# Kernel tuning notes

Hardware: AMD Instinct MI355X
Metric: run time of the kernel (lower is better)

Reference implementation:

```python
import jax, jax.numpy as jnp
import numpy as np
from jax import lax

B, C_IN, H, W = 4, 256, 64, 64
C_OUT = 512
KEY_DIM = C_OUT // 2   # 256
VAL_DIM = C_OUT // 2   # 256
HEADS = 8
EPS = 1e-5


def _conv(x, w, stride, pad):
    return lax.conv_general_dilated(
        x, w, (stride, stride), [(pad, pad), (pad, pad)],
        dimension_numbers=('NCHW', 'OIHW', 'NCHW'))


def setup_inputs() -> dict:
    key = jax.random.key(0)
    ks = jax.random.split(key, 10)
    x = jax.random.normal(ks[0], (B, C_IN, H, W), jnp.float32)
    bn_gamma = jax.random.uniform(ks[1], (C_IN,), jnp.float32, 0.5, 1.5)
    bn_beta = jax.random.normal(ks[2], (C_IN,), jnp.float32) * 0.1
    bn_mean = jax.random.normal(ks[3], (C_IN,), jnp.float32) * 0.1
    bn_var = jax.random.uniform(ks[4], (C_IN,), jnp.float32, 0.5, 1.5)
    w_short = jax.random.normal(ks[5], (C_OUT, C_IN, 3, 3), jnp.float32) * (1.0 / np.sqrt(C_IN * 9))
    wq = jax.random.normal(ks[6], (KEY_DIM, C_IN, 1, 1), jnp.float32) * (1.0 / np.sqrt(C_IN))
    wk = jax.random.normal(ks[7], (KEY_DIM, C_IN, 1, 1), jnp.float32) * (1.0 / np.sqrt(C_IN))
    wv = jax.random.normal(ks[8], (VAL_DIM, C_IN, 1, 1), jnp.float32) * (1.0 / np.sqrt(C_IN))
    wo = jax.random.normal(ks[9], (C_OUT, VAL_DIM, 1, 1), jnp.float32) * (1.0 / np.sqrt(VAL_DIM))
    return dict(x=x, bn_gamma=bn_gamma, bn_beta=bn_beta, bn_mean=bn_mean,
                bn_var=bn_var, w_short=w_short, wq=wq, wk=wk, wv=wv, wo=wo)


def reference(x, bn_gamma, bn_beta, bn_mean, bn_var, w_short, wq, wk, wv, wo):
    # BatchNorm (inference: running stats) + ReLU, fused elementwise chain
    inv = bn_gamma / jnp.sqrt(bn_var + EPS)
    h = jax.nn.relu((x - bn_mean[None, :, None, None]) * inv[None, :, None, None]
                    + bn_beta[None, :, None, None])

    # Projection shortcut: 3x3 conv, stride 2, pad 1, no bias -> [B, C_OUT, H/2, W/2]
    shortcut = _conv(h, w_short, 2, 1)

    # DOWN attention: queries at stride 2 (downsampled grid), keys/values at full res
    q = _conv(h, wq, 2, 0)   # [B, KEY_DIM, H/2, W/2]
    k = _conv(h, wk, 1, 0)   # [B, KEY_DIM, H, W]
    v = _conv(h, wv, 1, 0)   # [B, VAL_DIM, H, W]

    Ho, Wo = H // 2, W // 2
    dk = KEY_DIM // HEADS
    dv = VAL_DIM // HEADS
    Nq, Nk = Ho * Wo, H * W

    qh = q.reshape(B, HEADS, dk, Nq)
    kh = k.reshape(B, HEADS, dk, Nk)
    vh = v.reshape(B, HEADS, dv, Nk)

    scale = 1.0 / np.sqrt(dk)
    scores = jnp.einsum('bhdq,bhdk->bhqk', qh, kh) * scale  # [B,H,Nq,Nk]
    attn = jax.nn.softmax(scores, axis=-1)                  # use_softmax=True
    out = jnp.einsum('bhqk,bhdk->bhdq', attn, vh)           # [B,H,dv,Nq]
    out = out.reshape(B, VAL_DIM, Ho, Wo)
    out = _conv(out, wo, 1, 0)                              # [B, C_OUT, Ho, Wo]

    return shortcut + out
```

## Files before the change

### kernel.cpp

```cpp
#include <hip/hip_runtime.h>

#define BB    4
#define CIN   256
#define NPIX  4096
#define COUT  512
#define KD    256
#define HEADS 8
#define NQ    1024
#define NK    4096
#define EPSV  1e-5f
#define QSCALE (0.17677669529663687f * 1.4426950408889634f)

using short8 = __attribute__((ext_vector_type(8))) short;
using f32x4  = __attribute__((ext_vector_type(4))) float;

__device__ __forceinline__ float b2f(unsigned u){ return __uint_as_float(u << 16); }
__device__ __forceinline__ unsigned short f2b(float f){
  unsigned u = __float_as_uint(f);
  return (unsigned short)((u + 0x7fffu + ((u >> 16) & 1u)) >> 16);
}
__device__ __forceinline__ float bnrelu(float xv, float inv, float mu, float bt){
  return fmaxf((xv - mu) * inv + bt, 0.0f);
}
__device__ __forceinline__ unsigned pkbf(float lo, float hi){
  unsigned a = __float_as_uint(lo) + 0x8000u;
  unsigned b = __float_as_uint(hi) + 0x8000u;
  return __builtin_amdgcn_perm(b, a, 0x07060302u);
}
__device__ __forceinline__ unsigned cvtpk(float lo, float hi){
  unsigned r;
  asm("v_cvt_pk_bf16_f32 %0, %1, %2" : "=v"(r) : "v"(lo), "v"(hi));
  return r;
}

#define WF_K  2560
#define WF_E  (512*2560)

__global__ __launch_bounds__(256) void prep_all(
    const float* __restrict__ x, const float* __restrict__ gam,
    const float* __restrict__ bet, const float* __restrict__ mea,
    const float* __restrict__ var,
    const float* __restrict__ wsh, const float* __restrict__ wq,
    const float* __restrict__ wk,  const float* __restrict__ wv,
    const float* __restrict__ wo,
    unsigned short* __restrict__ h_t, unsigned short* __restrict__ W2){
  __shared__ unsigned short T[64][264];
  const int blk = blockIdx.x;
  const int t = threadIdx.x;
  if (blk < 832){
    if (blk < 512){
      float* R = (float*)&T[0][0];
      const float* src = wsh + (size_t)blk * 2304;
      #pragma unroll
      for (int i = 0; i < 9; ++i) R[i * 256 + t] = src[i * 256 + t];
      __syncthreads();
      unsigned short* dst = W2 + (size_t)blk * WF_K;
      #pragma unroll
      for (int i = 0; i < 9; ++i){
        int kp = i * 256 + t;
        int tap = kp >> 8, ci = kp & 255;
        dst[kp] = f2b(R[ci * 9 + tap]);
      }
    } else if (blk < 704){
      int idx = (blk - 512) * 1024 + t * 4;
      float4 v;
      if (idx < 65536){
        v = *(const float4*)(wq + idx);
        v.x *= QSCALE; v.y *= QSCALE; v.z *= QSCALE; v.w *= QSCALE;
      } else if (idx < 2*65536){ v = *(const float4*)(wk + idx - 65536);
      } else {                   v = *(const float4*)(wv + idx - 2*65536); }
      uint2 pk;
      pk.x = (unsigned)f2b(v.x) | ((unsigned)f2b(v.y) << 16);
      pk.y = (unsigned)f2b(v.z) | ((unsigned)f2b(v.w) << 16);
      *(uint2*)(W2 + WF_E + idx) = pk;
    } else {
      int idx = (blk - 704) * 1024 + t * 4;
      int m = idx >> 8, c = idx & 255;
      float4 v = *(const float4*)(wo + idx);
      uint2 pk;
      pk.x = (unsigned)f2b(v.x) | ((unsigned)f2b(v.y) << 16);
      pk.y = (unsigned)f2b(v.z) | ((unsigned)f2b(v.w) << 16);
      *(uint2*)(W2 + (size_t)m * WF_K + 2304 + c) = pk;
    }
    return;
  }
  const int lin = blk - 832;
  const int b = lin >> 6;
  const int pix0 = (lin & 63) * 64;
  const int w = t >> 6, lane = t & 63;
  for (int cc = 0; cc < 32; ++cc){
    int c0 = cc * 8 + w * 2;
    float i0 = gam[c0]   * rsqrtf(var[c0]   + EPSV), mu0 = mea[c0],   bt0 = bet[c0];
    float i1 = gam[c0+1] * rsqrtf(var[c0+1] + EPSV), mu1 = mea[c0+1], bt1 = bet[c0+1];
    float v0 = bnrelu(x[((size_t)(b*CIN + c0  ))*NPIX + pix0 + lane], i0, mu0, bt0);
    float v1 = bnrelu(x[((size_t)(b*CIN + c0+1))*NPIX + pix0 + lane], i1, mu1, bt1);
    *(unsigned*)&T[lane][c0] = pkbf(v0, v1);
  }
  __syncthreads();
  int p = t >> 2;
  unsigned short* dst = h_t + ((size_t)b * NPIX + pix0 + p) * CIN;
  #pragma unroll
  for (int i = 0; i < 8; ++i){
    int coff = i * 32 + (t & 3) * 8;
    *(uint4*)(dst + coff) = *(const uint4*)&T[p][coff];
  }
}

__global__ __launch_bounds__(256) void qkv_gemm(
    const unsigned short* __restrict__ Wkv,
    const unsigned short* __restrict__ Wq,
    const unsigned short* __restrict__ h_t,
    unsigned short* __restrict__ ktg,
    unsigned short* __restrict__ vtg,
    unsigned short* __restrict__ qt){
  __shared__ unsigned short As[64][72];
  __shared__ unsigned short Bs[128][72];
  const int b = blockIdx.z;
  const int t = threadIdx.x;
  const int w = t >> 6, lane = t & 63, col = lane & 15, quad = lane >> 4;
  const int wm = w & 1, wn = w >> 1;

  if (blockIdx.y < 8){
    const int m0 = blockIdx.y * 64;
    const bool isv = m0 >= 256;
    const int n0 = blockIdx.x * 128;
    f32x4 acc[2][4];
    #pragma unroll
    for (int i = 0; i < 2; ++i)
      #pragma unroll
      for (int j = 0; j < 4; ++j) acc[i][j] = (f32x4){0.f,0.f,0.f,0.f};
    const int am = t >> 2, ak = (t & 3) * 8;
    const int bn = t >> 1, bkh = (t & 1) * 16;
    const size_t browbase = ((size_t)b * NPIX + (n0 + bn)) * CIN;

    uint4 av0 = *(const uint4*)(Wkv + (size_t)(m0 + am) * 256 + ak);
    uint4 av1 = *(const uint4*)(Wkv + (size_t)(m0 + am) * 256 + 32 + ak);
    uint4 bv0 = *(const uint4*)(h_t + browbase + bkh);
    uint4 bv1 = *(const uint4*)(h_t + browbase + bkh + 8);
    uint4 bv2 = *(const uint4*)(h_t + browbase + 32 + bkh);
    uint4 bv3 = *(const uint4*)(h_t + browbase + 32 + bkh + 8);

    for (int k0 = 0; k0 < 256; k0 += 64){
      *(uint4*)&As[am][ak]           = av0;
      *(uint4*)&As[am][32 + ak]      = av1;
      *(uint4*)&Bs[bn][bkh]          = bv0;
      *(uint4*)&Bs[bn][bkh + 8]      = bv1;
      *(uint4*)&Bs[bn][32 + bkh]     = bv2;
      *(uint4*)&Bs[bn][32 + bkh + 8] = bv3;
      __syncthreads();
      if (k0 + 64 < 256){
        av0 = *(const uint4*)(Wkv + (size_t)(m0 + am) * 256 + k0 + 64 + ak);
        av1 = *(const uint4*)(Wkv + (size_t)(m0 + am) * 256 + k0 + 96 + ak);
        bv0 = *(const uint4*)(h_t + browbase + k0 + 64 + bkh);
        bv1 = *(const uint4*)(h_t + browbase + k0 + 64 + bkh + 8);
        bv2 = *(const uint4*)(h_t + browbase + k0 + 96 + bkh);
        bv3 = *(const uint4*)(h_t + browbase + k0 + 96 + bkh + 8);
      }
      #pragma unroll
      for (int h = 0; h < 2; ++h){
        short8 af[2], bf[4];
        af[0] = *(const short8*)&As[wm * 32 +      col][h * 32 + quad * 8];
        af[1] = *(const short8*)&As[wm * 32 + 16 + col][h * 32 + quad * 8];
        #pragma unroll
        for (int j = 0; j < 4; ++j)
          bf[j] = *(const short8*)&Bs[wn * 64 + j * 16 + col][h * 32 + quad * 8];
        if (!isv){
          #pragma unroll
          for (int i = 0; i < 2; ++i)
            #pragma unroll
            for (int j = 0; j < 4; ++j)
              acc[i][j] = __builtin_amdgcn_mfma_f32_16x16x32_bf16(af[i], bf[j], acc[i][j], 0, 0, 0);
        } else {
          #pragma unroll
          for (int i = 0; i < 2; ++i)
            #pragma unroll
            for (int j = 0; j < 4; ++j)
              acc[i][j] = __builtin_amdgcn_mfma_f32_16x16x32_bf16(bf[j], af[i], acc[i][j], 0, 0, 0);
        }
      }
      __syncthreads();
    }

    if (!isv){
      int head = (m0 + wm * 32) >> 5;
      #pragma unroll
      for (int i = 0; i < 2; ++i){
        int d0 = i * 16 + quad * 4;
        #pragma unroll
        for (int j = 0; j < 4; ++j){
          int n = n0 + wn * 64 + j * 16 + col;
          uint2 pk;
          pk.x = pkbf(acc[i][j][0], acc[i][j][1]);
          pk.y = pkbf(acc[i][j][2], acc[i][j][3]);
          *(uint2*)(ktg + ((size_t)(b * HEADS + head) * NK + n) * 32 + d0) = pk;
        }
      }
    } else {
      int head = ((m0 - 256) + wm * 32) >> 5;
      #pragma unroll
      for (int i = 0; i < 2; ++i){
        int d = i * 16 + col;
        #pragma unroll
        for (int j = 0; j < 4; ++j){
          int nb = n0 + wn * 64 + j * 16 + quad * 4;
          size_t addr = (((size_t)(b * HEADS + head) * 128 + (nb >> 5)) * 32 + d) * 32 + (nb & 31);
          uint2 pk;
          pk.x = pkbf(acc[i][j][0], acc[i][j][1]);
          pk.y = pkbf(acc[i][j][2], acc[i][j][3]);
          *(uint2*)(vtg + addr) = pk;
        }
      }
    }
    return;
  }

  const int lin = (blockIdx.y - 8) * 32 + blockIdx.x;
  const int m0 = (lin >> 4) * 64;
  const int n0 = (lin & 15) * 64;
  f32x4 acc[2][2];
  #pragma unroll
  for (int i = 0; i < 2; ++i)
    #pragma unroll
    for (int j = 0; j < 2; ++j) acc[i][j] = (f32x4){0.f,0.f,0.f,0.f};
  const int am = t >> 2, ak = (t & 3) * 8;
  const int bn = t >> 2, bk = (t & 3) * 8;
  int n = n0 + bn;
  const size_t browbase = ((size_t)b * NPIX + (((n >> 5) << 7) + ((n & 31) << 1))) * CIN;

  uint4 av0 = *(const uint4*)(Wq + (size_t)(m0 + am) * 256 + ak);
  uint4 av1 = *(const uint4*)(Wq + (size_t)(m0 + am) * 256 + 32 + ak);
  uint4 bv0 = *(const uint4*)(h_t + browbase + bk);
  uint4 bv1 = *(const uint4*)(h_t + browbase + 32 + bk);

  for (int k0 = 0; k0 < 256; k0 += 64){
    *(uint4*)&As[am][ak]      = av0;
    *(uint4*)&As[am][32 + ak] = av1;
    *(uint4*)&Bs[bn][bk]      = bv0;
    *(uint4*)&Bs[bn][32 + bk] = bv1;
    __syncthreads();
    if (k0 + 64 < 256){
      av0 = *(const uint4*)(Wq + (size_t)(m0 + am) * 256 + k0 + 64 + ak);
      av1 = *(const uint4*)(Wq + (size_t)(m0 + am) * 256 + k0 + 96 + ak);
      bv0 = *(const uint4*)(h_t + browbase + k0 + 64 + bk);
      bv1 = *(const uint4*)(h_t + browbase + k0 + 96 + bk);
    }
    #pragma unroll
    for (int h = 0; h < 2; ++h){
      short8 af[2], bf[2];
      af[0] = *(const short8*)&As[wm * 32 +      col][h * 32 + quad * 8];
      af[1] = *(const short8*)&As[wm * 32 + 16 + col][h * 32 + quad * 8];
      bf[0] = *(const short8*)&Bs[wn * 32 +      col][h * 32 + quad * 8];
      bf[1] = *(const short8*)&Bs[wn * 32 + 16 + col][h * 32 + quad * 8];
      #pragma unroll
      for (int i = 0; i < 2; ++i)
        #pragma unroll
        for (int j = 0; j < 2; ++j)
          acc[i][j] = __builtin_amdgcn_mfma_f32_16x16x32_bf16(af[i], bf[j], acc[i][j], 0, 0, 0);
    }
    __syncthreads();
  }

  int head = (m0 + wm * 32) >> 5;
  #pragma unroll
  for (int i = 0; i < 2; ++i){
    int d0 = i * 16 + quad * 4;
    #pragma unroll
    for (int j = 0; j < 2; ++j){
      int nn = n0 + wn * 32 + j * 16 + col;
      uint2 pk;
      pk.x = pkbf(acc[i][j][0], acc[i][j][1]);
      pk.y = pkbf(acc[i][j][2], acc[i][j][3]);
      *(uint2*)(qt + ((size_t)(b * HEADS + head) * NQ + nn) * 32 + d0) = pk;
    }
  }
}

__global__ __launch_bounds__(256) void scwo_gemm(
    const unsigned short* __restrict__ Wf,
    const unsigned short* __restrict__ h_t,
    const unsigned short* __restrict__ aot,
    float* __restrict__ outf){
  const int b  = blockIdx.z;
  const int m0 = blockIdx.y * 64;
  const int n0 = blockIdx.x * 64;
  const int t  = threadIdx.x;
  const int w = t >> 6, lane = t & 63, col = lane & 15, quad = lane >> 4;
  const int wm = w & 1, wn = w >> 1;
  __shared__ unsigned short As[64][72];
  __shared__ unsigned short Bs[64][72];
  f32x4 acc[2][2];
  #pragma unroll
  for (int i = 0; i < 2; ++i)
    #pragma unroll
    for (int j = 0; j < 2; ++j) acc[i][j] = (f32x4){0.f,0.f,0.f,0.f};
  const int am = t >> 2, ak = (t & 3) * 8;
  const int bn = t >> 2, bk = (t & 3) * 8;
  const int n = n0 + bn;
  const int oy = n >> 5, ox = n & 31;
  const size_t aobase = ((size_t)b * NQ + n) * KD;

  auto loadB = [&](int k0) -> uint4 {
    if (k0 < 2304){
      int tap = k0 >> 8;
      int ky = tap / 3, kx = tap - ky * 3;
      int iy = 2 * oy + ky - 1, ix = 2 * ox + kx - 1;
      if (((unsigned)iy < 64u) && ((unsigned)ix < 64u))
        return *(const uint4*)(h_t + ((size_t)b * NPIX + iy * 64 + ix) * CIN + (k0 & 255) + bk);
      return make_uint4(0,0,0,0);
    }
    return *(const uint4*)(aot + aobase + (k0 - 2304) + bk);
  };

  uint4 av0 = *(const uint4*)(Wf + (size_t)(m0 + am) * WF_K + ak);
  uint4 av1 = *(const uint4*)(Wf + (size_t)(m0 + am) * WF_K + 32 + ak);
  uint4 bv0 = loadB(0);
  uint4 bv1 = loadB(32);

  for (int k0 = 0; k0 < WF_K; k0 += 64){
    *(uint4*)&As[am][ak]      = av0;
    *(uint4*)&As[am][32 + ak] = av1;
    *(uint4*)&Bs[bn][bk]      = bv0;
    *(uint4*)&Bs[bn][32 + bk] = bv1;
    __syncthreads();
    if (k0 + 64 < WF_K){
      av0 = *(const uint4*)(Wf + (size_t)(m0 + am) * WF_K + k0 + 64 + ak);
      av1 = *(const uint4*)(Wf + (size_t)(m0 + am) * WF_K + k0 + 96 + ak);
      bv0 = loadB(k0 + 64);
      bv1 = loadB(k0 + 96);
    }
    #pragma unroll
    for (int h = 0; h < 2; ++h){
      short8 af[2], bf[2];
      af[0] = *(const short8*)&As[wm * 32 +      col][h * 32 + quad * 8];
      af[1] = *(const short8*)&As[wm * 32 + 16 + col][h * 32 + quad * 8];
      bf[0] = *(const short8*)&Bs[wn * 32 +      col][h * 32 + quad * 8];
      bf[1] = *(const short8*)&Bs[wn * 32 + 16 + col][h * 32 + quad * 8];
      #pragma unroll
      for (int i = 0; i < 2; ++i)
        #pragma unroll
        for (int j = 0; j < 2; ++j)
          acc[i][j] = __builtin_amdgcn_mfma_f32_16x16x32_bf16(bf[j], af[i], acc[i][j], 0, 0, 0);
    }
    __syncthreads();
  }

  #pragma unroll
  for (int i = 0; i < 2; ++i){
    int co = m0 + wm * 32 + i * 16 + col;
    #pragma unroll
    for (int j = 0; j < 2; ++j){
      int nb = n0 + wn * 32 + j * 16 + quad * 4;
      float4 o;
      o.x = acc[i][j][0]; o.y = acc[i][j][1];
      o.z = acc[i][j][2]; o.w = acc[i][j][3];
      *(float4*)(outf + ((size_t)(b * COUT + co)) * NQ + nb) = o;
    }
  }
}

__global__ __launch_bounds__(512) void attn12(
    const unsigned short* __restrict__ qt,
    const unsigned short* __restrict__ ktg,
    const unsigned short* __restrict__ vtg,
    float* __restrict__ po,
    float* __restrict__ pl){
  __shared__ unsigned short KV[2][8192];
  const int bid = blockIdx.x;
  const int xcd = bid & 7, idx = bid >> 3;
  const int bh = xcd * 4 + (idx & 3);
  const int qg = (idx >> 2) & 7;
  const int kh = idx >> 5;
  const int t = threadIdx.x;
  const int w = t >> 6, lane = t & 63, col = lane & 15, quad = lane >> 4;
  const int q = (qg * 8 + w) * 16 + col;

  short8 qf = *(const short8*)(qt + ((size_t)bh * NQ + q) * 32 + quad * 8);
  const unsigned short* kb = ktg + (size_t)bh * NK * 32;
  const unsigned short* vb = vtg + (size_t)bh * 128 * 1024;

  const int sg = (w & 3) >> 1, sf = w & 1;
  const size_t ksrc = (size_t)(32 * sg + 16 * sf + col) * 32 + quad * 8;
  const size_t vsrc = (size_t)sg * 1024 + (size_t)(16 * sf + col) * 32 + quad * 8;
  const unsigned short* sb = ((w < 4) ? kb + ksrc : vb + vsrc) + (size_t)kh * 65536;
  unsigned short* ddst = &KV[0][w * 512 + lane * 8 + ((w < 4) ? 0 : 2048)];

  f32x4 O0 = {0.f,0.f,0.f,0.f}, O1 = {0.f,0.f,0.f,0.f}, l4 = {0.f,0.f,0.f,0.f};
  const short8 ones = {0x3F80,0x3F80,0x3F80,0x3F80,0x3F80,0x3F80,0x3F80,0x3F80};

  *(uint4*)ddst          = *(const uint4*)sb;
  *(uint4*)(ddst + 2048) = *(const uint4*)(sb + 2048);
  __syncthreads();

  for (int s = 0; s < 16; ++s){
    const int cur = s & 1;
    uint4 n1, n2;
    if (s + 1 < 16){
      size_t soff = (size_t)(s + 1) * 4096;
      n1 = *(const uint4*)(sb + soff);
      n2 = *(const uint4*)(sb + soff + 2048);
    }
    #pragma unroll
    for (int g = 0; g < 4; ++g){
      const unsigned short* Kp = &KV[cur][g * 1024];
      short8 kf0 = *(const short8*)(Kp +       lane * 8);
      short8 kf1 = *(const short8*)(Kp + 512 + lane * 8);
      f32x4 z = {0.f,0.f,0.f,0.f};
      f32x4 slo = __builtin_amdgcn_mfma_f32_16x16x32_bf16(kf0, qf, z, 0, 0, 0);
      f32x4 shi = __builtin_amdgcn_mfma_f32_16x16x32_bf16(kf1, qf, z, 0, 0, 0);

      unsigned x0 = cvtpk(__builtin_amdgcn_exp2f(slo[0]), __builtin_amdgcn_exp2f(slo[1]));
      unsigned x1 = cvtpk(__builtin_amdgcn_exp2f(slo[2]), __builtin_amdgcn_exp2f(slo[3]));
      unsigned y0 = cvtpk(__builtin_amdgcn_exp2f(shi[0]), __builtin_amdgcn_exp2f(shi[1]));
      unsigned y1 = cvtpk(__builtin_amdgcn_exp2f(shi[2]), __builtin_amdgcn_exp2f(shi[3]));
      asm("v_permlane32_swap_b32 %0, %1" : "+v"(x0), "+v"(y0));
      asm("v_permlane32_swap_b32 %0, %1" : "+v"(x1), "+v"(y1));
      asm("v_permlane16_swap_b32 %0, %1" : "+v"(x0), "+v"(y0));
      asm("v_permlane16_swap_b32 %0, %1" : "+v"(x1), "+v"(y1));
      unsigned f[4] = {x0, x1, y0, y1};
      short8 pf;
      memcpy(&pf, f, 16);

      const unsigned short* Vp = &KV[cur][4096 + g * 1024];
      short8 vf0 = *(const short8*)(Vp +       lane * 8);
      short8 vf1 = *(const short8*)(Vp + 512 + lane * 8);
      O0 = __builtin_amdgcn_mfma_f32_16x16x32_bf16(vf0, pf, O0, 0, 0, 0);
      O1 = __builtin_amdgcn_mfma_f32_16x16x32_bf16(vf1, pf, O1, 0, 0, 0);
      l4 = __builtin_amdgcn_mfma_f32_16x16x32_bf16(ones, pf, l4, 0, 0, 0);
    }
    if (s + 1 < 16){
      *(uint4*)(ddst + (size_t)(cur ^ 1) * 8192)        = n1;
      *(uint4*)(ddst + 2048 + (size_t)(cur ^ 1) * 8192) = n2;
    }
    __syncthreads();
  }

  float* pob = po + (((size_t)(kh * 32 + bh) * NQ + q) * 32);
  *(f32x4*)(pob + quad * 4)      = O0;
  *(f32x4*)(pob + 16 + quad * 4) = O1;
  if (quad == 0) pl[(size_t)(kh * 32 + bh) * NQ + q] = l4[0];
}

__global__ __launch_bounds__(256) void attn_merge(
    const float* __restrict__ po, const float* __restrict__ pl,
    unsigned short* __restrict__ aot){
  const int g = blockIdx.x * 256 + threadIdx.x;
  const int pair = g >> 1, half = g & 1;
  const int bh = pair >> 10, q = pair & 1023;
  const int b = bh >> 3, hd = bh & 7;
  const float* p0 = po + ((size_t)bh * NQ + q) * 32 + half * 16;
  const float* p1 = p0 + (size_t)32 * NQ * 32;
  float l = pl[(size_t)bh * NQ + q] + pl[(size_t)(32 + bh) * NQ + q];
  float inv = 1.0f / l;
  float o[16];
  #pragma unroll
  for (int i = 0; i < 16; i += 4){
    float4 a = *(const float4*)(p0 + i);
    float4 c = *(const float4*)(p1 + i);
    o[i]   = (a.x + c.x) * inv;
    o[i+1] = (a.y + c.y) * inv;
    o[i+2] = (a.z + c.z) * inv;
    o[i+3] = (a.w + c.w) * inv;
  }
  unsigned short* dst = aot + ((size_t)(b * NQ + q)) * KD + hd * 32 + half * 16;
  uint4 pk;
  pk.x = pkbf(o[0],  o[1]);  pk.y = pkbf(o[2],  o[3]);
  pk.z = pkbf(o[4],  o[5]);  pk.w = pkbf(o[6],  o[7]);
  *(uint4*)dst = pk;
  pk.x = pkbf(o[8],  o[9]);  pk.y = pkbf(o[10], o[11]);
  pk.z = pkbf(o[12], o[13]); pk.w = pkbf(o[14], o[15]);
  *(uint4*)(dst + 8) = pk;
}

extern "C" void kernel_launch(void* const* d_in, const int* in_sizes, int n_in,
                              void* d_out, int out_size, void* d_ws, size_t ws_size,
                              hipStream_t stream){
  const float* x   = (const float*)d_in[0];
  const float* bg  = (const float*)d_in[1];
  const float* bbt = (const float*)d_in[2];
  const float* bm  = (const float*)d_in[3];
  const float* bv  = (const float*)d_in[4];
  const float* wsh = (const float*)d_in[5];
  const float* wq  = (const float*)d_in[6];
  const float* wk  = (const float*)d_in[7];
  const float* wvv = (const float*)d_in[8];
  const float* wo  = (const float*)d_in[9];
  float* out = (float*)d_out;

  unsigned short* h_t = (unsigned short*)d_ws;
  unsigned short* W2  = h_t + (size_t)BB * NPIX * CIN;
  unsigned short* qt  = W2  + (WF_E + 3*65536);
  unsigned short* aot = qt  + (size_t)BB * HEADS * NQ * 32;
  unsigned short* ktg = aot + (size_t)BB * NQ * KD;
  unsigned short* vtg = ktg + (size_t)BB * HEADS * NK * 32;
  unsigned short* wend = vtg + (size_t)BB * HEADS * 32 * NK;
  float* po = (float*)wend;
  float* pl = po + (size_t)2 * 32 * NQ * 32;
  size_t need = ((size_t)(wend - h_t)) * 2
              + ((size_t)2 * 32 * NQ * 32 + (size_t)2 * 32 * NQ) * 4;
  if (ws_size < need) return;

  unsigned short* Wf   = W2;
  unsigned short* wq2  = W2 + WF_E;
  unsigned short* wkv2 = wq2 + 65536;

  prep_all<<<dim3(1088), dim3(256), 0, stream>>>(x, bg, bbt, bm, bv,
                                                 wsh, wq, wk, wvv, wo, h_t, W2);
  qkv_gemm<<<dim3(32, 10, 4), dim3(256), 0, stream>>>(wkv2, wq2, h_t, ktg, vtg, qt);
  attn12<<<dim3(512), dim3(512), 0, stream>>>(qt, ktg, vtg, po, pl);
  attn_merge<<<dim3(256), dim3(256), 0, stream>>>(po, pl, aot);
  scwo_gemm<<<dim3(16, 8, 4), dim3(256), 0, stream>>>(Wf, h_t, aot, out);
}
```

Measured before the change: 165.0 us.

## Process two query tiles per wave and split keys four ways in attention

Each wave now computes two 16-query tiles against each K/V tile staged in shared memory, so every LDS load of K and V is reused twice. The key dimension is split into four chunks instead of two, which keeps the block count at 512. The merge kernel now sums four partial outputs and four partial denominators. The cost is more registers per wave (a launch-bounds hint asks for 4 blocks) and twice the partial-result traffic to and from global memory.

```diff
diff --git a/kernel.cpp b/kernel.cpp
--- a/kernel.cpp
+++ b/kernel.cpp
@@ -358,7 +358,7 @@
   }
 }
 
-__global__ __launch_bounds__(512) void attn12(
+__global__ __launch_bounds__(512, 4) void attn13(
     const unsigned short* __restrict__ qt,
     const unsigned short* __restrict__ ktg,
     const unsigned short* __restrict__ vtg,
@@ -368,33 +368,36 @@
   const int bid = blockIdx.x;
   const int xcd = bid & 7, idx = bid >> 3;
   const int bh = xcd * 4 + (idx & 3);
-  const int qg = (idx >> 2) & 7;
-  const int kh = idx >> 5;
+  const int qg = (idx >> 2) & 3;
+  const int kh = idx >> 4;
   const int t = threadIdx.x;
   const int w = t >> 6, lane = t & 63, col = lane & 15, quad = lane >> 4;
-  const int q = (qg * 8 + w) * 16 + col;
-
-  short8 qf = *(const short8*)(qt + ((size_t)bh * NQ + q) * 32 + quad * 8);
+  const int qA = (qg * 16 + 2 * w) * 16 + col;
+  const int qB = qA + 16;
+
+  short8 qfA = *(const short8*)(qt + ((size_t)bh * NQ + qA) * 32 + quad * 8);
+  short8 qfB = *(const short8*)(qt + ((size_t)bh * NQ + qB) * 32 + quad * 8);
   const unsigned short* kb = ktg + (size_t)bh * NK * 32;
   const unsigned short* vb = vtg + (size_t)bh * 128 * 1024;
 
   const int sg = (w & 3) >> 1, sf = w & 1;
   const size_t ksrc = (size_t)(32 * sg + 16 * sf + col) * 32 + quad * 8;
   const size_t vsrc = (size_t)sg * 1024 + (size_t)(16 * sf + col) * 32 + quad * 8;
-  const unsigned short* sb = ((w < 4) ? kb + ksrc : vb + vsrc) + (size_t)kh * 65536;
+  const unsigned short* sb = ((w < 4) ? kb + ksrc : vb + vsrc) + (size_t)kh * 32768;
   unsigned short* ddst = &KV[0][w * 512 + lane * 8 + ((w < 4) ? 0 : 2048)];
 
-  f32x4 O0 = {0.f,0.f,0.f,0.f}, O1 = {0.f,0.f,0.f,0.f}, l4 = {0.f,0.f,0.f,0.f};
+  f32x4 OA0 = {0.f,0.f,0.f,0.f}, OA1 = {0.f,0.f,0.f,0.f}, lA = {0.f,0.f,0.f,0.f};
+  f32x4 OB0 = {0.f,0.f,0.f,0.f}, OB1 = {0.f,0.f,0.f,0.f}, lB = {0.f,0.f,0.f,0.f};
   const short8 ones = {0x3F80,0x3F80,0x3F80,0x3F80,0x3F80,0x3F80,0x3F80,0x3F80};
 
   *(uint4*)ddst          = *(const uint4*)sb;
   *(uint4*)(ddst + 2048) = *(const uint4*)(sb + 2048);
   __syncthreads();
 
-  for (int s = 0; s < 16; ++s){
+  for (int s = 0; s < 8; ++s){
     const int cur = s & 1;
     uint4 n1, n2;
-    if (s + 1 < 16){
+    if (s + 1 < 8){
       size_t soff = (size_t)(s + 1) * 4096;
       n1 = *(const uint4*)(sb + soff);
       n2 = *(const uint4*)(sb + soff + 2048);
@@ -405,39 +408,62 @@
       short8 kf0 = *(const short8*)(Kp +       lane * 8);
       short8 kf1 = *(const short8*)(Kp + 512 + lane * 8);
       f32x4 z = {0.f,0.f,0.f,0.f};
-      f32x4 slo = __builtin_amdgcn_mfma_f32_16x16x32_bf16(kf0, qf, z, 0, 0, 0);
-      f32x4 shi = __builtin_amdgcn_mfma_f32_16x16x32_bf16(kf1, qf, z, 0, 0, 0);
-
-      unsigned x0 = cvtpk(__builtin_amdgcn_exp2f(slo[0]), __builtin_amdgcn_exp2f(slo[1]));
-      unsigned x1 = cvtpk(__builtin_amdgcn_exp2f(slo[2]), __builtin_amdgcn_exp2f(slo[3]));
-      unsigned y0 = cvtpk(__builtin_amdgcn_exp2f(shi[0]), __builtin_amdgcn_exp2f(shi[1]));
-      unsigned y1 = cvtpk(__builtin_amdgcn_exp2f(shi[2]), __builtin_amdgcn_exp2f(shi[3]));
-      asm("v_permlane32_swap_b32 %0, %1" : "+v"(x0), "+v"(y0));
-      asm("v_permlane32_swap_b32 %0, %1" : "+v"(x1), "+v"(y1));
-      asm("v_permlane16_swap_b32 %0, %1" : "+v"(x0), "+v"(y0));
-      asm("v_permlane16_swap_b32 %0, %1" : "+v"(x1), "+v"(y1));
-      unsigned f[4] = {x0, x1, y0, y1};
-      short8 pf;
-      memcpy(&pf, f, 16);
+      f32x4 sloA = __builtin_amdgcn_mfma_f32_16x16x32_bf16(kf0, qfA, z, 0, 0, 0);
+      f32x4 shiA = __builtin_amdgcn_mfma_f32_16x16x32_bf16(kf1, qfA, z, 0, 0, 0);
+      f32x4 sloB = __builtin_amdgcn_mfma_f32_16x16x32_bf16(kf0, qfB, z, 0, 0, 0);
+      f32x4 shiB = __builtin_amdgcn_mfma_f32_16x16x32_bf16(kf1, qfB, z, 0, 0, 0);
+
+      unsigned xa0 = cvtpk(__builtin_amdgcn_exp2f(sloA[0]), __builtin_amdgcn_exp2f(sloA[1]));
+      unsigned xa1 = cvtpk(__builtin_amdgcn_exp2f(sloA[2]), __builtin_amdgcn_exp2f(sloA[3]));
+      unsigned ya0 = cvtpk(__builtin_amdgcn_exp2f(shiA[0]), __builtin_amdgcn_exp2f(shiA[1]));
+      unsigned ya1 = cvtpk(__builtin_amdgcn_exp2f(shiA[2]), __builtin_amdgcn_exp2f(shiA[3]));
+      asm("v_permlane32_swap_b32 %0, %1" : "+v"(xa0), "+v"(ya0));
+      asm("v_permlane32_swap_b32 %0, %1" : "+v"(xa1), "+v"(ya1));
+      asm("v_permlane16_swap_b32 %0, %1" : "+v"(xa0), "+v"(ya0));
+      asm("v_permlane16_swap_b32 %0, %1" : "+v"(xa1), "+v"(ya1));
+      unsigned fa[4] = {xa0, xa1, ya0, ya1};
+      short8 pfA;
+      memcpy(&pfA, fa, 16);
+
+      unsigned xb0 = cvtpk(__builtin_amdgcn_exp2f(sloB[0]), __builtin_amdgcn_exp2f(sloB[1]));
+      unsigned xb1 = cvtpk(__builtin_amdgcn_exp2f(sloB[2]), __builtin_amdgcn_exp2f(sloB[3]));
+      unsigned yb0 = cvtpk(__builtin_amdgcn_exp2f(shiB[0]), __builtin_amdgcn_exp2f(shiB[1]));
+      unsigned yb1 = cvtpk(__builtin_amdgcn_exp2f(shiB[2]), __builtin_amdgcn_exp2f(shiB[3]));
+      asm("v_permlane32_swap_b32 %0, %1" : "+v"(xb0), "+v"(yb0));
+      asm("v_permlane32_swap_b32 %0, %1" : "+v"(xb1), "+v"(yb1));
+      asm("v_permlane16_swap_b32 %0, %1" : "+v"(xb0), "+v"(yb0));
+      asm("v_permlane16_swap_b32 %0, %1" : "+v"(xb1), "+v"(yb1));
+      unsigned fb[4] = {xb0, xb1, yb0, yb1};
+      short8 pfB;
+      memcpy(&pfB, fb, 16);
 
       const unsigned short* Vp = &KV[cur][4096 + g * 1024];
       short8 vf0 = *(const short8*)(Vp +       lane * 8);
       short8 vf1 = *(const short8*)(Vp + 512 + lane * 8);
-      O0 = __builtin_amdgcn_mfma_f32_16x16x32_bf16(vf0, pf, O0, 0, 0, 0);
-      O1 = __builtin_amdgcn_mfma_f32_16x16x32_bf16(vf1, pf, O1, 0, 0, 0);
-      l4 = __builtin_amdgcn_mfma_f32_16x16x32_bf16(ones, pf, l4, 0, 0, 0);
-    }
-    if (s + 1 < 16){
+      OA0 = __builtin_amdgcn_mfma_f32_16x16x32_bf16(vf0, pfA, OA0, 0, 0, 0);
+      OA1 = __builtin_amdgcn_mfma_f32_16x16x32_bf16(vf1, pfA, OA1, 0, 0, 0);
+      lA  = __builtin_amdgcn_mfma_f32_16x16x32_bf16(ones, pfA, lA, 0, 0, 0);
+      OB0 = __builtin_amdgcn_mfma_f32_16x16x32_bf16(vf0, pfB, OB0, 0, 0, 0);
+      OB1 = __builtin_amdgcn_mfma_f32_16x16x32_bf16(vf1, pfB, OB1, 0, 0, 0);
+      lB  = __builtin_amdgcn_mfma_f32_16x16x32_bf16(ones, pfB, lB, 0, 0, 0);
+    }
+    if (s + 1 < 8){
       *(uint4*)(ddst + (size_t)(cur ^ 1) * 8192)        = n1;
       *(uint4*)(ddst + 2048 + (size_t)(cur ^ 1) * 8192) = n2;
     }
     __syncthreads();
   }
 
-  float* pob = po + (((size_t)(kh * 32 + bh) * NQ + q) * 32);
-  *(f32x4*)(pob + quad * 4)      = O0;
-  *(f32x4*)(pob + 16 + quad * 4) = O1;
-  if (quad == 0) pl[(size_t)(kh * 32 + bh) * NQ + q] = l4[0];
+  float* pA = po + (((size_t)(kh * 32 + bh) * NQ + qA) * 32);
+  *(f32x4*)(pA + quad * 4)      = OA0;
+  *(f32x4*)(pA + 16 + quad * 4) = OA1;
+  float* pB = po + (((size_t)(kh * 32 + bh) * NQ + qB) * 32);
+  *(f32x4*)(pB + quad * 4)      = OB0;
+  *(f32x4*)(pB + 16 + quad * 4) = OB1;
+  if (quad == 0){
+    pl[(size_t)(kh * 32 + bh) * NQ + qA] = lA[0];
+    pl[(size_t)(kh * 32 + bh) * NQ + qB] = lB[0];
+  }
 }
 
 __global__ __launch_bounds__(256) void attn_merge(
@@ -447,19 +473,24 @@
   const int pair = g >> 1, half = g & 1;
   const int bh = pair >> 10, q = pair & 1023;
   const int b = bh >> 3, hd = bh & 7;
+  const size_t KH = (size_t)32 * NQ * 32;
   const float* p0 = po + ((size_t)bh * NQ + q) * 32 + half * 16;
-  const float* p1 = p0 + (size_t)32 * NQ * 32;
-  float l = pl[(size_t)bh * NQ + q] + pl[(size_t)(32 + bh) * NQ + q];
+  float l = pl[(size_t)bh * NQ + q]
+          + pl[(size_t)(32 + bh) * NQ + q]
+          + pl[(size_t)(64 + bh) * NQ + q]
+          + pl[(size_t)(96 + bh) * NQ + q];
   float inv = 1.0f / l;
   float o[16];
   #pragma unroll
   for (int i = 0; i < 16; i += 4){
     float4 a = *(const float4*)(p0 + i);
-    float4 c = *(const float4*)(p1 + i);
-    o[i]   = (a.x + c.x) * inv;
-    o[i+1] = (a.y + c.y) * inv;
-    o[i+2] = (a.z + c.z) * inv;
-    o[i+3] = (a.w + c.w) * inv;
+    float4 c = *(const float4*)(p0 + KH + i);
+    float4 d = *(const float4*)(p0 + 2 * KH + i);
+    float4 e = *(const float4*)(p0 + 3 * KH + i);
+    o[i]   = (a.x + c.x + d.x + e.x) * inv;
+    o[i+1] = (a.y + c.y + d.y + e.y) * inv;
+    o[i+2] = (a.z + c.z + d.z + e.z) * inv;
+    o[i+3] = (a.w + c.w + d.w + e.w) * inv;
   }
   unsigned short* dst = aot + ((size_t)(b * NQ + q)) * KD + hd * 32 + half * 16;
   uint4 pk;
@@ -494,9 +525,9 @@
   unsigned short* vtg = ktg + (size_t)BB * HEADS * NK * 32;
   unsigned short* wend = vtg + (size_t)BB * HEADS * 32 * NK;
   float* po = (float*)wend;
-  float* pl = po + (size_t)2 * 32 * NQ * 32;
+  float* pl = po + (size_t)4 * 32 * NQ * 32;
   size_t need = ((size_t)(wend - h_t)) * 2
-              + ((size_t)2 * 32 * NQ * 32 + (size_t)2 * 32 * NQ) * 4;
+              + ((size_t)4 * 32 * NQ * 32 + (size_t)4 * 32 * NQ) * 4;
   if (ws_size < need) return;
 
   unsigned short* Wf   = W2;
@@ -506,7 +537,7 @@
   prep_all<<<dim3(1088), dim3(256), 0, stream>>>(x, bg, bbt, bm, bv,
                                                  wsh, wq, wk, wvv, wo, h_t, W2);
   qkv_gemm<<<dim3(32, 10, 4), dim3(256), 0, stream>>>(wkv2, wq2, h_t, ktg, vtg, qt);
-  attn12<<<dim3(512), dim3(512), 0, stream>>>(qt, ktg, vtg, po, pl);
+  attn13<<<dim3(512), dim3(512), 0, stream>>>(qt, ktg, vtg, po, pl);
   attn_merge<<<dim3(256), dim3(256), 0, stream>>>(po, pl, aot);
   scwo_gemm<<<dim3(16, 8, 4), dim3(256), 0, stream>>>(Wf, h_t, aot, out);
 }
```

Measured after the change: 166.8 us. About the same (+1.1%).
